# Optimization experiments

Measured on AMD Instinct MI355X. Metric: run time of the kernel, lower is better.

## Reference

```python
import jax, jax.numpy as jnp
import numpy as np

GAMMA = 1.4
EX = jnp.array([1.0, 0.0], dtype=jnp.float32)
EY = jnp.array([0.0, 1.0], dtype=jnp.float32)


def _mlp(x, Ws, bs):
    h = x
    for W, b in zip(Ws[:-1], bs[:-1]):
        h = jnp.tanh(h @ W + b)
    return h @ Ws[-1] + bs[-1]


def setup_inputs() -> dict:
    key = jax.random.key(0)
    ks = jax.random.split(key, 24)
    N, NB = 32768, 4096
    inp = {}
    dom = jnp.array([1.5, 1.0], dtype=jnp.float32)
    inp['x_train'] = jax.random.uniform(ks[0], (N, 2), dtype=jnp.float32) * dom
    inp['x_inlet'] = jax.random.uniform(ks[1], (NB, 2), dtype=jnp.float32) * dom
    inp['U_inlet'] = jax.random.normal(ks[2], (NB, 4), dtype=jnp.float32)
    inp['x_base'] = jax.random.uniform(ks[3], (NB, 2), dtype=jnp.float32) * dom
    inp['x_top'] = jax.random.uniform(ks[4], (NB, 2), dtype=jnp.float32) * dom
    inp['x_slipNormal'] = jax.random.uniform(ks[5], (NB, 2), dtype=jnp.float32) * dom
    dims = [2, 128, 128, 128, 128, 4]
    for i in range(5):
        fan_in = dims[i]
        inp[f'W{i}'] = jax.random.normal(ks[6 + i], (dims[i], dims[i + 1]), dtype=jnp.float32) / jnp.sqrt(jnp.float32(fan_in))
        inp[f'b{i}'] = jnp.zeros((dims[i + 1],), dtype=jnp.float32)
    d2 = [2, 64, 64, 1]
    for i in range(3):
        inp[f'V{i}'] = jax.random.normal(ks[12 + i], (d2[i], d2[i + 1]), dtype=jnp.float32) / jnp.sqrt(jnp.float32(d2[i]))
        inp[f'c{i}'] = jnp.zeros((d2[i + 1],), dtype=jnp.float32)
    return inp


def reference(x_train, x_inlet, U_inlet, x_base, x_top, x_slipNormal,
              W0, b0, W1, b1, W2, b2, W3, b3, W4, b4,
              V0, c0, V1, c1, V2, c2):
    Ws = [W0, W1, W2, W3, W4]
    bs = [b0, b1, b2, b3, b4]
    Vs = [V0, V1, V2]
    cs = [c0, c1, c2]

    def fields(xy):
        # per-point: returns [U1..U4, f1..f4, g1..g4] (12,)
        rho, p, u, v = _mlp(xy, Ws, bs)
        E = p / (GAMMA - 1.0) + 0.5 * rho * (u * u + v * v)
        return jnp.stack([
            rho, rho * u, rho * v, E,                               # U
            rho * u, rho * u * u + p, rho * u * v, u * (E + p),     # f (x-flux)
            rho * v, rho * u * v, rho * v * v + p, v * (E + p)])    # g (y-flux)

    def dUx(xy):
        return jax.jvp(fields, (xy,), (EX,))[1][:4]

    def dUy(xy):
        return jax.jvp(fields, (xy,), (EY,))[1][:4]

    def point_residual(xy):
        _, dx = jax.jvp(fields, (xy,), (EX,))   # x-derivs of all 12 fields
        _, dy = jax.jvp(fields, (xy,), (EY,))   # y-derivs
        U_xx = jax.jvp(dUx, (xy,), (EX,))[1]    # second derivs (fwd-over-fwd)
        U_yy = jax.jvp(dUy, (xy,), (EY,))[1]
        mu = 0.01 * _mlp(xy, Vs, cs)[0] ** 2
        res = dx[4:8] + dy[8:12] - mu * (U_xx + U_yy)  # (4,)
        return res, mu

    res, mu = jax.vmap(point_residual)(x_train)  # res: (N,4), mu: (N,)
    physics = jnp.sum(jnp.mean(res ** 2, axis=0))  # r1+r2+r3+r4

    out_in = _mlp(x_inlet, Ws, bs)
    inlet = jnp.sum(jnp.mean((out_in - U_inlet) ** 2, axis=0))

    base = jnp.mean(_mlp(x_base, Ws, bs)[:, 3] ** 2)
    top = jnp.mean(_mlp(x_top, Ws, bs)[:, 3] ** 2)

    ang = -jnp.pi / 18.0
    o = _mlp(x_slipNormal, Ws, bs)
    slip = jnp.mean((-o[:, 2] * jnp.sin(ang) + o[:, 3] * jnp.cos(ang)) ** 2)

    total = physics + 10.0 * (inlet + base + top + slip) + 0.1 * jnp.mean(mu ** 2)
    return total
```

## Files before the change

### kernel.cpp

```cpp
#include <hip/hip_runtime.h>

#define NTRAIN 32768
#define NBDY   4096
#define PHYS_BLOCKS (NTRAIN / 32)
#define BDY_BLOCKS  256

typedef _Float16 f16x8 __attribute__((ext_vector_type(8)));
typedef __fp16   fp16x2 __attribute__((ext_vector_type(2)));
typedef float    f32x4 __attribute__((ext_vector_type(4)));

union FragU { uint4 q; f16x8 b; _Float16 e[8]; };
union F4  { float4 v; float f[4]; };
union U2h { _Float16 e[4]; uint2 d; };
union H2  { fp16x2 h; _Float16 e[2]; unsigned int u; };

__device__ __forceinline__ float fast_tanh(float z) {
    float e = __expf(2.0f * z);
    return 1.0f - 2.0f * __builtin_amdgcn_rcpf(e + 1.0f);
}

__device__ __forceinline__ unsigned int pk2(float a, float b) {
    H2 r; r.h = __builtin_amdgcn_cvt_pkrtz(a, b);
    return r.u;
}

__global__ __launch_bounds__(256) void pack_w_kernel(
    const float* __restrict__ W1, const float* __restrict__ W2,
    const float* __restrict__ W3, const float* __restrict__ V1,
    const float* __restrict__ W4,
    unsigned short* __restrict__ wsU, float* __restrict__ out)
{
    int b = blockIdx.x;
    if (b < 24) {
        int mat = b >> 3, rb = b & 7;
        const float* W = (mat == 0) ? W1 : (mat == 1) ? W2 : W3;
        unsigned int* hiU = (unsigned int*)(wsU + mat * 32768);
        unsigned int* loU = hiU + 8192;
        int n   = threadIdx.x & 127;
        int pr0 = threadIdx.x >> 7;
        #pragma unroll
        for (int it = 0; it < 4; it++) {
            int pr = pr0 + 2 * it;
            int k  = rb * 16 + pr * 2;
            float v0 = W[k * 128 + n];
            float v1 = W[(k + 1) * 128 + n];
            H2 hh, ll;
            hh.e[0] = (_Float16)v0;
            hh.e[1] = (_Float16)v1;
            ll.e[0] = (_Float16)(v0 - (float)hh.e[0]);
            ll.e[1] = (_Float16)(v1 - (float)hh.e[1]);
            int base = ((n >> 4) * 4 + (k >> 5)) * 64 + ((k >> 3) & 3) * 16 + (n & 15);
            int uoff = base * 4 + ((k & 7) >> 1);
            hiU[uoff] = hh.u;
            loU[uoff] = ll.u;
        }
    } else if (b == 24) {
        unsigned int* hiU = (unsigned int*)(wsU + 98304);
        int n   = threadIdx.x & 63;
        int pr0 = threadIdx.x >> 6;
        #pragma unroll
        for (int it = 0; it < 8; it++) {
            int pr = pr0 + 4 * it;
            int k  = pr * 2;
            float v0 = V1[k * 64 + n];
            float v1 = V1[(k + 1) * 64 + n];
            H2 hh;
            hh.e[0] = (_Float16)v0;
            hh.e[1] = (_Float16)v1;
            int base = ((n >> 4) * 2 + (k >> 5)) * 64 + ((k >> 3) & 3) * 16 + (n & 15);
            hiU[base * 4 + ((k & 7) >> 1)] = hh.u;
        }
        if (threadIdx.x == 0) out[0] = 0.f;
    } else {
        _Float16* hi = (_Float16*)(wsU + 102400);
        _Float16* lo = hi + 2048;
        int u4 = threadIdx.x;
        int lane = u4 & 63, ks = u4 >> 6;
        int m  = lane & 15;
        int kb = ks * 32 + ((lane >> 4) << 3);
        FragU fh, fl;
        #pragma unroll
        for (int j = 0; j < 8; j++) {
            float v = (m < 4) ? W4[(kb + j) * 4 + m] : 0.f;
            _Float16 h = (_Float16)v;
            fh.e[j] = h;
            fl.e[j] = (_Float16)(v - (float)h);
        }
        *(uint4*)(hi + u4 * 8) = fh.q;
        *(uint4*)(lo + u4 * 8) = fl.q;
    }
}

__global__ __launch_bounds__(256, 4) void fused_kernel(
    const float* __restrict__ xt,
    const float* __restrict__ x_inlet, const float* __restrict__ U_inlet,
    const float* __restrict__ x_base,  const float* __restrict__ x_top,
    const float* __restrict__ x_slip,
    const float* __restrict__ W0, const float* __restrict__ b0,
    const float* __restrict__ W1, const float* __restrict__ b1,
    const float* __restrict__ W2, const float* __restrict__ b2,
    const float* __restrict__ W3, const float* __restrict__ b3,
    const float* __restrict__ W4, const float* __restrict__ b4,
    const float* __restrict__ V0, const float* __restrict__ c0,
    const float* __restrict__ V1, const float* __restrict__ c1,
    const float* __restrict__ V2, const float* __restrict__ c2,
    const unsigned short* __restrict__ wsU,
    float* __restrict__ out)
{
    __shared__ float SM[9664];
    const int t = threadIdx.x;
    const int wv   = t >> 6;
    const int lane = t & 63;
    const int nn   = lane & 15;
    const int q    = lane >> 4;

    if (blockIdx.x < PHYS_BLOCKS) {
        unsigned short* AhU = (unsigned short*)SM;
        float* OUTF   = SM + 8704;
        float* MUPART = SM + 9216;
        float* BIASF  = SM + 9280;

        if (t < 128) {
            BIASF[t]       = b1[t];
            BIASF[128 + t] = b2[t];
            BIASF[256 + t] = b3[t];
        }

        {
            const int g = wv >> 1, h = wv & 1;
            const float2 xyn = *(const float2*)(xt + (blockIdx.x * 32 + g * 16 + nn) * 2);
            FragU mb[2];
            #pragma unroll
            for (int ks = 0; ks < 2; ks++) {
                int u0 = ks * 32 + q * 8;
                F4 va0, va1, vb0, vb1, cc0, cc1;
                va0.v = *(const float4*)(V0 + u0);
                va1.v = *(const float4*)(V0 + u0 + 4);
                vb0.v = *(const float4*)(V0 + 64 + u0);
                vb1.v = *(const float4*)(V0 + 64 + u0 + 4);
                cc0.v = *(const float4*)(c0 + u0);
                cc1.v = *(const float4*)(c0 + u0 + 4);
                #pragma unroll
                for (int i = 0; i < 4; i++) {
                    mb[ks].e[i]     = (_Float16)fast_tanh(
                        xyn.x * va0.f[i] + xyn.y * vb0.f[i] + cc0.f[i]);
                    mb[ks].e[4 + i] = (_Float16)fast_tanh(
                        xyn.x * va1.f[i] + xyn.y * vb1.f[i] + cc1.f[i]);
                }
            }
            float partial = 0.f;
            #pragma unroll
            for (int i = 0; i < 2; i++) {
                f32x4 macc = {0.f, 0.f, 0.f, 0.f};
                #pragma unroll
                for (int ks = 0; ks < 2; ks++) {
                    FragU vh;
                    vh.q = *(const uint4*)(wsU + 98304 +
                           ((((2 * h + i) * 2 + ks) * 64 + lane) << 3));
                    macc = __builtin_amdgcn_mfma_f32_16x16x32_f16(vh.b, mb[ks].b, macc, 0, 0, 0);
                }
                int u2 = (2 * h + i) * 16 + q * 4;
                F4 cv, w2;
                cv.v = *(const float4*)(c1 + u2);
                w2.v = *(const float4*)(V2 + u2);
                #pragma unroll
                for (int r = 0; r < 4; r++)
                    partial += fast_tanh(macc[r] + cv.f[r]) * w2.f[r];
            }
            partial += __shfl_xor(partial, 16);
            partial += __shfl_xor(partial, 32);
            if (lane < 16) MUPART[wv * 16 + nn] = partial;
        }
        {
            const int pl = t >> 4, c = t & 15;
            #pragma unroll
            for (int h = 0; h < 2; h++) {
                const int p = h * 16 + pl;
                const float2 xy = *(const float2*)(xt + (blockIdx.x * 32 + p) * 2);
                const float x = xy.x, y = xy.y;
                float vals[4][8];
                #pragma unroll
                for (int j = 0; j < 8; j++) {
                    int u = c * 8 + j;
                    float w0 = W0[u], w1 = W0[128 + u];
                    float zv = x * w0 + y * w1 + b0[u];
                    float tt = fast_tanh(zv);
                    float s2 = 1.f - tt * tt;
                    float m2 = -2.f * tt * s2;
                    vals[0][j] = tt;
                    vals[1][j] = s2 * w0;
                    vals[2][j] = s2 * w1;
                    vals[3][j] = m2 * (w0 * w0 + w1 * w1);
                }
                #pragma unroll
                for (int s = 0; s < 4; s++) {
                    uint4 d = make_uint4(pk2(vals[s][0], vals[s][1]),
                                         pk2(vals[s][2], vals[s][3]),
                                         pk2(vals[s][4], vals[s][5]),
                                         pk2(vals[s][6], vals[s][7]));
                    *(uint4*)(AhU + ((h * 4 + s) * 16 + pl) * 136 + c * 8) = d;
                }
            }
        }
        __syncthreads();

        #pragma unroll 1
        for (int l = 0; l < 3; l++) {
            const unsigned short* WpL = wsU + l * 32768;
            f32x4 acc[2][8];
            #pragma unroll
            for (int i = 0; i < 2; i++)
                #pragma unroll
                for (int s = 0; s < 8; s++) {
                    acc[i][s][0] = 0.f; acc[i][s][1] = 0.f;
                    acc[i][s][2] = 0.f; acc[i][s][3] = 0.f;
                }
            #pragma unroll
            for (int ks = 0; ks < 4; ks++) {
                FragU wh[2];
                #pragma unroll
                for (int i = 0; i < 2; i++)
                    wh[i].q = *(const uint4*)(WpL + ((((2 * wv + i) * 4 + ks) * 64 + lane) << 3));
                #pragma unroll
                for (int s = 0; s < 8; s++) {
                    FragU bh;
                    bh.q = *(const uint4*)(AhU + (s * 16 + nn) * 136 + ks * 32 + q * 8);
                    acc[0][s] = __builtin_amdgcn_mfma_f32_16x16x32_f16(
                        wh[0].b, bh.b, acc[0][s], 0, 0, 0);
                    acc[1][s] = __builtin_amdgcn_mfma_f32_16x16x32_f16(
                        wh[1].b, bh.b, acc[1][s], 0, 0, 0);
                }
            }
            __syncthreads();
            #pragma unroll
            for (int i = 0; i < 2; i++) {
                const int ubase = (2 * wv + i) * 16 + q * 4;
                F4 bv; bv.v = *(const float4*)&BIASF[l * 128 + ubase];
                #pragma unroll
                for (int g = 0; g < 2; g++) {
                    float vals[4][4];
                    #pragma unroll
                    for (int r = 0; r < 4; r++) {
                        float z  = acc[i][g * 4 + 0][r] + bv.f[r];
                        float zx = acc[i][g * 4 + 1][r];
                        float zy = acc[i][g * 4 + 2][r];
                        float zl = acc[i][g * 4 + 3][r];
                        float tt = fast_tanh(z);
                        float s2 = 1.f - tt * tt;
                        float m2 = -2.f * tt * s2;
                        vals[0][r] = tt;
                        vals[1][r] = s2 * zx;
                        vals[2][r] = s2 * zy;
                        vals[3][r] = s2 * zl + m2 * (zx * zx + zy * zy);
                    }
                    #pragma unroll
                    for (int s = 0; s < 4; s++) {
                        uint2 d = make_uint2(pk2(vals[s][0], vals[s][1]),
                                             pk2(vals[s][2], vals[s][3]));
                        *(uint2*)(AhU + ((g * 4 + s) * 16 + nn) * 136 + ubase) = d;
                    }
                }
            }
            __syncthreads();
        }

        {
            const unsigned short* W4p = wsU + 102400;
            #pragma unroll
            for (int g = 0; g < 2; g++) {
                const int rt = g * 4 + wv;
                f32x4 a4 = {0.f, 0.f, 0.f, 0.f};
                #pragma unroll
                for (int ks = 0; ks < 4; ks++) {
                    FragU bh, wh, wl;
                    bh.q = *(const uint4*)(AhU + (rt * 16 + nn) * 136 + ks * 32 + q * 8);
                    const unsigned short* base = W4p + ((ks * 64 + lane) << 3);
                    wh.q = *(const uint4*)base;
                    wl.q = *(const uint4*)(base + 2048);
                    a4 = __builtin_amdgcn_mfma_f32_16x16x32_f16(wh.b, bh.b, a4, 0, 0, 0);
                    a4 = __builtin_amdgcn_mfma_f32_16x16x32_f16(wl.b, bh.b, a4, 0, 0, 0);
                }
                if (q == 0) {
                    float4 o = make_float4(a4[0], a4[1], a4[2], a4[3]);
                    if (wv == 0) {
                        o.x += b4[0]; o.y += b4[1]; o.z += b4[2]; o.w += b4[3];
                    }
                    *(float4*)&OUTF[(rt * 16 + nn) * 4] = o;
                }
            }
        }
        __syncthreads();

        float contrib = 0.f;
        if (t < 32) {
            const int pp = t, g = pp >> 4, p15 = pp & 15;
            const float* V   = &OUTF[((g * 4 + 0) * 16 + p15) * 4];
            const float* DX  = &OUTF[((g * 4 + 1) * 16 + p15) * 4];
            const float* DY  = &OUTF[((g * 4 + 2) * 16 + p15) * 4];
            const float* LAP = &OUTF[((g * 4 + 3) * 16 + p15) * 4];
            float r = V[0],  P = V[1],  u = V[2],  v = V[3];
            float rx = DX[0], Px = DX[1], ux = DX[2], vx = DX[3];
            float ry = DY[0], Py = DY[1], uy = DY[2], vy = DY[3];
            float rl = LAP[0], Pl = LAP[1], ul = LAP[2], vl = LAP[3];
            const float GI = 2.5f;

            float s = MUPART[g * 32 + p15] + MUPART[g * 32 + 16 + p15] + c2[0];
            float mu = 0.01f * s * s;

            float q2 = u * u + v * v;
            float E  = P * GI + 0.5f * r * q2;
            float Ex = Px * GI + 0.5f * rx * q2 + r * (u * ux + v * vx);
            float Ey = Py * GI + 0.5f * ry * q2 + r * (u * uy + v * vy);
            float EpP = E + P;

            float f1x = rx * u + r * ux;
            float f2x = rx * u * u + 2.f * r * u * ux + Px;
            float f3x = rx * u * v + r * ux * v + r * u * vx;
            float f4x = ux * EpP + u * (Ex + Px);

            float g1y = ry * v + r * vy;
            float g2y = ry * u * v + r * uy * v + r * u * vy;
            float g3y = ry * v * v + 2.f * r * v * vy + Py;
            float g4y = vy * EpP + v * (Ey + Py);

            float qx  = 2.f * (u * ux + v * vx);
            float qy  = 2.f * (u * uy + v * vy);
            float ql  = 2.f * (ux * ux + uy * uy + vx * vx + vy * vy)
                      + 2.f * (u * ul + v * vl);

            float U1s = rl;
            float U2s = rl * u + 2.f * (rx * ux + ry * uy) + r * ul;
            float U3s = rl * v + 2.f * (rx * vx + ry * vy) + r * vl;
            float U4s = Pl * GI
                      + 0.5f * (rl * q2 + 2.f * (rx * qx + ry * qy) + r * ql);

            float r1 = f1x + g1y - mu * U1s;
            float r2 = f2x + g2y - mu * U2s;
            float r3 = f3x + g3y - mu * U3s;
            float r4 = f4x + g4y - mu * U4s;

            contrib = (r1 * r1 + r2 * r2 + r3 * r3 + r4 * r4 + 0.1f * mu * mu)
                      * (1.0f / (float)NTRAIN);
        }
        if (t < 64) {
            contrib += __shfl_down(contrib, 32);
            contrib += __shfl_down(contrib, 16);
            contrib += __shfl_down(contrib, 8);
            contrib += __shfl_down(contrib, 4);
            contrib += __shfl_down(contrib, 2);
            contrib += __shfl_down(contrib, 1);
            if (t == 0) atomicAdd(out, contrib);
        }
    } else {
        unsigned short* ShU = (unsigned short*)SM;
        float* OUTB  = SM + 4352;
        float* BIASB = SM + 4608;

        const int bb    = blockIdx.x - PHYS_BLOCKS;
        const int batch = bb >> 6;
        const int lb    = bb & 63;
        const float* xs = (batch == 0) ? x_inlet
                        : (batch == 1) ? x_base
                        : (batch == 2) ? x_top : x_slip;
        const int base_pt = lb * 64;

        {
            int p2 = t & 63, ug = t >> 6;
            float2 xy = *(const float2*)(xs + (base_pt + p2) * 2);
            float x = xy.x, y = xy.y;
            #pragma unroll
            for (int g = 0; g < 8; g++) {
                int u0 = ug * 32 + g * 4;
                F4 wa, wb, bbv;
                wa.v  = *(const float4*)(W0 + u0);
                wb.v  = *(const float4*)(W0 + 128 + u0);
                bbv.v = *(const float4*)(b0 + u0);
                float t0 = fast_tanh(x * wa.f[0] + y * wb.f[0] + bbv.f[0]);
                float t1 = fast_tanh(x * wa.f[1] + y * wb.f[1] + bbv.f[1]);
                float t2 = fast_tanh(x * wa.f[2] + y * wb.f[2] + bbv.f[2]);
                float t3 = fast_tanh(x * wa.f[3] + y * wb.f[3] + bbv.f[3]);
                uint2 d = make_uint2(pk2(t0, t1), pk2(t2, t3));
                *(uint2*)(ShU + p2 * 136 + u0) = d;
            }
            if (t < 128) {
                BIASB[t]       = b1[t];
                BIASB[128 + t] = b2[t];
                BIASB[256 + t] = b3[t];
            }
        }
        __syncthreads();

        #pragma unroll 1
        for (int l = 0; l < 3; l++) {
            const unsigned short* WpL = wsU + l * 32768;
            f32x4 acc[2][4];
            #pragma unroll
            for (int i = 0; i < 2; i++)
                #pragma unroll
                for (int n = 0; n < 4; n++) {
                    acc[i][n][0] = 0.f; acc[i][n][1] = 0.f;
                    acc[i][n][2] = 0.f; acc[i][n][3] = 0.f;
                }
            #pragma unroll
            for (int ks = 0; ks < 4; ks++) {
                FragU bh[4];
                #pragma unroll
                for (int n = 0; n < 4; n++)
                    bh[n].q = *(const uint4*)(ShU + (n * 16 + nn) * 136 + ks * 32 + q * 8);
                FragU wh[2];
                #pragma unroll
                for (int i = 0; i < 2; i++)
                    wh[i].q = *(const uint4*)(WpL + ((((2 * wv + i) * 4 + ks) * 64 + lane) << 3));
                #pragma unroll
                for (int i = 0; i < 2; i++)
                    #pragma unroll
                    for (int n = 0; n < 4; n++)
                        acc[i][n] = __builtin_amdgcn_mfma_f32_16x16x32_f16(
                            wh[i].b, bh[n].b, acc[i][n], 0, 0, 0);
            }
            __syncthreads();
            #pragma unroll
            for (int i = 0; i < 2; i++) {
                int ubase = (2 * wv + i) * 16 + q * 4;
                F4 bv; bv.v = *(const float4*)&BIASB[l * 128 + ubase];
                #pragma unroll
                for (int n = 0; n < 4; n++) {
                    float t0 = fast_tanh(acc[i][n][0] + bv.f[0]);
                    float t1 = fast_tanh(acc[i][n][1] + bv.f[1]);
                    float t2 = fast_tanh(acc[i][n][2] + bv.f[2]);
                    float t3 = fast_tanh(acc[i][n][3] + bv.f[3]);
                    uint2 d = make_uint2(pk2(t0, t1), pk2(t2, t3));
                    *(uint2*)(ShU + (n * 16 + nn) * 136 + ubase) = d;
                }
            }
            __syncthreads();
        }

        {
            const unsigned short* W4p = wsU + 102400;
            f32x4 a4 = {0.f, 0.f, 0.f, 0.f};
            #pragma unroll
            for (int ks = 0; ks < 4; ks++) {
                FragU bh, wh, wl;
                bh.q = *(const uint4*)(ShU + (wv * 16 + nn) * 136 + ks * 32 + q * 8);
                const unsigned short* base = W4p + ((ks * 64 + lane) << 3);
                wh.q = *(const uint4*)base;
                wl.q = *(const uint4*)(base + 2048);
                a4 = __builtin_amdgcn_mfma_f32_16x16x32_f16(wh.b, bh.b, a4, 0, 0, 0);
                a4 = __builtin_amdgcn_mfma_f32_16x16x32_f16(wl.b, bh.b, a4, 0, 0, 0);
            }
            if (q == 0) {
                float4 o = make_float4(a4[0] + b4[0], a4[1] + b4[1],
                                       a4[2] + b4[2], a4[3] + b4[3]);
                *(float4*)&OUTB[(wv * 16 + nn) * 4] = o;
            }
        }
        __syncthreads();

        float contrib = 0.f;
        if (t < 64) {
            float o0 = OUTB[t * 4 + 0], o1 = OUTB[t * 4 + 1];
            float o2 = OUTB[t * 4 + 2], o3 = OUTB[t * 4 + 3];
            float l;
            if (batch == 0) {
                float4 Ui = *(const float4*)(U_inlet + (base_pt + t) * 4);
                float d0 = o0 - Ui.x, d1 = o1 - Ui.y, d2 = o2 - Ui.z, d3 = o3 - Ui.w;
                l = d0 * d0 + d1 * d1 + d2 * d2 + d3 * d3;
            } else if (batch == 3) {
                const float sa = -0.17364817766693033f;
                const float ca =  0.9848077530122080f;
                float d = -o2 * sa + o3 * ca;
                l = d * d;
            } else {
                l = o3 * o3;
            }
            contrib = 10.0f * l * (1.0f / (float)NBDY);
        }
        if (t < 64) {
            contrib += __shfl_down(contrib, 32);
            contrib += __shfl_down(contrib, 16);
            contrib += __shfl_down(contrib, 8);
            contrib += __shfl_down(contrib, 4);
            contrib += __shfl_down(contrib, 2);
            contrib += __shfl_down(contrib, 1);
            if (t == 0) atomicAdd(out, contrib);
        }
    }
}

extern "C" void kernel_launch(void* const* d_in, const int* in_sizes, int n_in,
                              void* d_out, int out_size, void* d_ws, size_t ws_size,
                              hipStream_t stream) {
    const float* xt      = (const float*)d_in[0];
    const float* x_inlet = (const float*)d_in[1];
    const float* U_inlet = (const float*)d_in[2];
    const float* x_base  = (const float*)d_in[3];
    const float* x_top   = (const float*)d_in[4];
    const float* x_slip  = (const float*)d_in[5];
    const float* W0 = (const float*)d_in[6];
    const float* b0 = (const float*)d_in[7];
    const float* W1 = (const float*)d_in[8];
    const float* b1 = (const float*)d_in[9];
    const float* W2 = (const float*)d_in[10];
    const float* b2 = (const float*)d_in[11];
    const float* W3 = (const float*)d_in[12];
    const float* b3 = (const float*)d_in[13];
    const float* W4 = (const float*)d_in[14];
    const float* b4 = (const float*)d_in[15];
    const float* V0 = (const float*)d_in[16];
    const float* c0 = (const float*)d_in[17];
    const float* V1 = (const float*)d_in[18];
    const float* c1 = (const float*)d_in[19];
    const float* V2 = (const float*)d_in[20];
    const float* c2 = (const float*)d_in[21];
    float* out = (float*)d_out;
    unsigned short* wsU = (unsigned short*)d_ws;

    pack_w_kernel<<<26, 256, 0, stream>>>(W1, W2, W3, V1, W4, wsU, out);

    fused_kernel<<<PHYS_BLOCKS + BDY_BLOCKS, 256, 0, stream>>>(
        xt, x_inlet, U_inlet, x_base, x_top, x_slip,
        W0, b0, W1, b1, W2, b2, W3, b3, W4, b4,
        V0, c0, V1, c1, V2, c2, wsU, out);
}
```

Before: 132.8 us.

## Double block size to 512 threads with 64 points and per-wave weight ownership

```diff
diff --git a/kernel.cpp b/kernel.cpp
--- a/kernel.cpp
+++ b/kernel.cpp
@@ -2,8 +2,10 @@
 
 #define NTRAIN 32768
 #define NBDY   4096
-#define PHYS_BLOCKS (NTRAIN / 32)
-#define BDY_BLOCKS  256
+#define PHYS_BLOCKS (NTRAIN / 64)
+#define BDY_BLOCKS  128
+
+#define LDS_BYTES 71680
 
 typedef _Float16 f16x8 __attribute__((ext_vector_type(8)));
 typedef __fp16   fp16x2 __attribute__((ext_vector_type(2)));
@@ -11,7 +13,6 @@
 
 union FragU { uint4 q; f16x8 b; _Float16 e[8]; };
 union F4  { float4 v; float f[4]; };
-union U2h { _Float16 e[4]; uint2 d; };
 union H2  { fp16x2 h; _Float16 e[2]; unsigned int u; };
 
 __device__ __forceinline__ float fast_tanh(float z) {
@@ -91,7 +92,7 @@
     }
 }
 
-__global__ __launch_bounds__(256, 4) void fused_kernel(
+__global__ __launch_bounds__(512, 4) void fused_kernel(
     const float* __restrict__ xt,
     const float* __restrict__ x_inlet, const float* __restrict__ U_inlet,
     const float* __restrict__ x_base,  const float* __restrict__ x_top,
@@ -107,7 +108,11 @@
     const unsigned short* __restrict__ wsU,
     float* __restrict__ out)
 {
-    __shared__ float SM[9664];
+    extern __shared__ char SMC[];
+    unsigned short* AhU = (unsigned short*)SMC;
+    float* MUPART = (float*)(SMC + 69632);
+    float* BIASF  = (float*)(SMC + 70144);
+
     const int t = threadIdx.x;
     const int wv   = t >> 6;
     const int lane = t & 63;
@@ -115,10 +120,7 @@
     const int q    = lane >> 4;
 
     if (blockIdx.x < PHYS_BLOCKS) {
-        unsigned short* AhU = (unsigned short*)SM;
-        float* OUTF   = SM + 8704;
-        float* MUPART = SM + 9216;
-        float* BIASF  = SM + 9280;
+        const int blk = blockIdx.x;
 
         if (t < 128) {
             BIASF[t]       = b1[t];
@@ -128,7 +130,7 @@
 
         {
             const int g = wv >> 1, h = wv & 1;
-            const float2 xyn = *(const float2*)(xt + (blockIdx.x * 32 + g * 16 + nn) * 2);
+            const float2 xyn = *(const float2*)(xt + (blk * 64 + g * 16 + nn) * 2);
             FragU mb[2];
             #pragma unroll
             for (int ks = 0; ks < 2; ks++) {
@@ -174,9 +176,9 @@
         {
             const int pl = t >> 4, c = t & 15;
             #pragma unroll
-            for (int h = 0; h < 2; h++) {
-                const int p = h * 16 + pl;
-                const float2 xy = *(const float2*)(xt + (blockIdx.x * 32 + p) * 2);
+            for (int h2 = 0; h2 < 2; h2++) {
+                const int p = h2 * 32 + pl;
+                const float2 xy = *(const float2*)(xt + (blk * 64 + p) * 2);
                 const float x = xy.x, y = xy.y;
                 float vals[4][8];
                 #pragma unroll
@@ -192,13 +194,14 @@
                     vals[2][j] = s2 * w1;
                     vals[3][j] = m2 * (w0 * w0 + w1 * w1);
                 }
+                const int g = p >> 4, p15 = p & 15;
                 #pragma unroll
                 for (int s = 0; s < 4; s++) {
                     uint4 d = make_uint4(pk2(vals[s][0], vals[s][1]),
                                          pk2(vals[s][2], vals[s][3]),
                                          pk2(vals[s][4], vals[s][5]),
                                          pk2(vals[s][6], vals[s][7]));
-                    *(uint4*)(AhU + ((h * 4 + s) * 16 + pl) * 136 + c * 8) = d;
+                    *(uint4*)(AhU + ((g * 4 + s) * 16 + p15) * 136 + c * 8) = d;
                 }
             }
         }
@@ -207,58 +210,51 @@
         #pragma unroll 1
         for (int l = 0; l < 3; l++) {
             const unsigned short* WpL = wsU + l * 32768;
-            f32x4 acc[2][8];
-            #pragma unroll
-            for (int i = 0; i < 2; i++)
-                #pragma unroll
-                for (int s = 0; s < 8; s++) {
-                    acc[i][s][0] = 0.f; acc[i][s][1] = 0.f;
-                    acc[i][s][2] = 0.f; acc[i][s][3] = 0.f;
-                }
+            f32x4 acc[16];
+            #pragma unroll
+            for (int s = 0; s < 16; s++) {
+                acc[s][0] = 0.f; acc[s][1] = 0.f;
+                acc[s][2] = 0.f; acc[s][3] = 0.f;
+            }
+            FragU wh[4];
+            #pragma unroll
+            for (int ks = 0; ks < 4; ks++)
+                wh[ks].q = *(const uint4*)(WpL + (((wv * 4 + ks) * 64 + lane) << 3));
             #pragma unroll
             for (int ks = 0; ks < 4; ks++) {
-                FragU wh[2];
-                #pragma unroll
-                for (int i = 0; i < 2; i++)
-                    wh[i].q = *(const uint4*)(WpL + ((((2 * wv + i) * 4 + ks) * 64 + lane) << 3));
-                #pragma unroll
-                for (int s = 0; s < 8; s++) {
+                #pragma unroll
+                for (int s = 0; s < 16; s++) {
                     FragU bh;
                     bh.q = *(const uint4*)(AhU + (s * 16 + nn) * 136 + ks * 32 + q * 8);
-                    acc[0][s] = __builtin_amdgcn_mfma_f32_16x16x32_f16(
-                        wh[0].b, bh.b, acc[0][s], 0, 0, 0);
-                    acc[1][s] = __builtin_amdgcn_mfma_f32_16x16x32_f16(
-                        wh[1].b, bh.b, acc[1][s], 0, 0, 0);
+                    acc[s] = __builtin_amdgcn_mfma_f32_16x16x32_f16(
+                        wh[ks].b, bh.b, acc[s], 0, 0, 0);
                 }
             }
             __syncthreads();
-            #pragma unroll
-            for (int i = 0; i < 2; i++) {
-                const int ubase = (2 * wv + i) * 16 + q * 4;
-                F4 bv; bv.v = *(const float4*)&BIASF[l * 128 + ubase];
-                #pragma unroll
-                for (int g = 0; g < 2; g++) {
-                    float vals[4][4];
-                    #pragma unroll
-                    for (int r = 0; r < 4; r++) {
-                        float z  = acc[i][g * 4 + 0][r] + bv.f[r];
-                        float zx = acc[i][g * 4 + 1][r];
-                        float zy = acc[i][g * 4 + 2][r];
-                        float zl = acc[i][g * 4 + 3][r];
-                        float tt = fast_tanh(z);
-                        float s2 = 1.f - tt * tt;
-                        float m2 = -2.f * tt * s2;
-                        vals[0][r] = tt;
-                        vals[1][r] = s2 * zx;
-                        vals[2][r] = s2 * zy;
-                        vals[3][r] = s2 * zl + m2 * (zx * zx + zy * zy);
-                    }
-                    #pragma unroll
-                    for (int s = 0; s < 4; s++) {
-                        uint2 d = make_uint2(pk2(vals[s][0], vals[s][1]),
-                                             pk2(vals[s][2], vals[s][3]));
-                        *(uint2*)(AhU + ((g * 4 + s) * 16 + nn) * 136 + ubase) = d;
-                    }
+            const int ubase = wv * 16 + q * 4;
+            F4 bv; bv.v = *(const float4*)&BIASF[l * 128 + ubase];
+            #pragma unroll
+            for (int g = 0; g < 4; g++) {
+                float vals[4][4];
+                #pragma unroll
+                for (int r = 0; r < 4; r++) {
+                    float z  = acc[g * 4 + 0][r] + bv.f[r];
+                    float zx = acc[g * 4 + 1][r];
+                    float zy = acc[g * 4 + 2][r];
+                    float zl = acc[g * 4 + 3][r];
+                    float tt = fast_tanh(z);
+                    float s2 = 1.f - tt * tt;
+                    float m2 = -2.f * tt * s2;
+                    vals[0][r] = tt;
+                    vals[1][r] = s2 * zx;
+                    vals[2][r] = s2 * zy;
+                    vals[3][r] = s2 * zl + m2 * (zx * zx + zy * zy);
+                }
+                #pragma unroll
+                for (int s = 0; s < 4; s++) {
+                    uint2 d = make_uint2(pk2(vals[s][0], vals[s][1]),
+                                         pk2(vals[s][2], vals[s][3]));
+                    *(uint2*)(AhU + ((g * 4 + s) * 16 + nn) * 136 + ubase) = d;
                 }
             }
             __syncthreads();
@@ -266,45 +262,53 @@
 
         {
             const unsigned short* W4p = wsU + 102400;
-            #pragma unroll
-            for (int g = 0; g < 2; g++) {
-                const int rt = g * 4 + wv;
-                f32x4 a4 = {0.f, 0.f, 0.f, 0.f};
-                #pragma unroll
-                for (int ks = 0; ks < 4; ks++) {
-                    FragU bh, wh, wl;
-                    bh.q = *(const uint4*)(AhU + (rt * 16 + nn) * 136 + ks * 32 + q * 8);
-                    const unsigned short* base = W4p + ((ks * 64 + lane) << 3);
-                    wh.q = *(const uint4*)base;
-                    wl.q = *(const uint4*)(base + 2048);
-                    a4 = __builtin_amdgcn_mfma_f32_16x16x32_f16(wh.b, bh.b, a4, 0, 0, 0);
-                    a4 = __builtin_amdgcn_mfma_f32_16x16x32_f16(wl.b, bh.b, a4, 0, 0, 0);
-                }
-                if (q == 0) {
-                    float4 o = make_float4(a4[0], a4[1], a4[2], a4[3]);
-                    if (wv == 0) {
-                        o.x += b4[0]; o.y += b4[1]; o.z += b4[2]; o.w += b4[3];
-                    }
-                    *(float4*)&OUTF[(rt * 16 + nn) * 4] = o;
-                }
+            const int rtA = wv, rtB = 8 + wv;
+            f32x4 aA = {0.f, 0.f, 0.f, 0.f};
+            f32x4 aB = {0.f, 0.f, 0.f, 0.f};
+            #pragma unroll
+            for (int ks = 0; ks < 4; ks++) {
+                FragU wh, wl, bA, bB;
+                const unsigned short* base = W4p + ((ks * 64 + lane) << 3);
+                wh.q = *(const uint4*)base;
+                wl.q = *(const uint4*)(base + 2048);
+                bA.q = *(const uint4*)(AhU + (rtA * 16 + nn) * 136 + ks * 32 + q * 8);
+                bB.q = *(const uint4*)(AhU + (rtB * 16 + nn) * 136 + ks * 32 + q * 8);
+                aA = __builtin_amdgcn_mfma_f32_16x16x32_f16(wh.b, bA.b, aA, 0, 0, 0);
+                aA = __builtin_amdgcn_mfma_f32_16x16x32_f16(wl.b, bA.b, aA, 0, 0, 0);
+                aB = __builtin_amdgcn_mfma_f32_16x16x32_f16(wh.b, bB.b, aB, 0, 0, 0);
+                aB = __builtin_amdgcn_mfma_f32_16x16x32_f16(wl.b, bB.b, aB, 0, 0, 0);
+            }
+            if (q == 0) {
+                float4 oA = make_float4(aA[0], aA[1], aA[2], aA[3]);
+                float4 oB = make_float4(aB[0], aB[1], aB[2], aB[3]);
+                if ((rtA & 3) == 0) {
+                    oA.x += b4[0]; oA.y += b4[1]; oA.z += b4[2]; oA.w += b4[3];
+                }
+                if ((rtB & 3) == 0) {
+                    oB.x += b4[0]; oB.y += b4[1]; oB.z += b4[2]; oB.w += b4[3];
+                }
+                *(float4*)(SMC + (rtA * 16 + nn) * 272 + 256) = oA;
+                *(float4*)(SMC + (rtB * 16 + nn) * 272 + 256) = oB;
             }
         }
         __syncthreads();
 
         float contrib = 0.f;
-        if (t < 32) {
+        if (t < 64) {
             const int pp = t, g = pp >> 4, p15 = pp & 15;
-            const float* V   = &OUTF[((g * 4 + 0) * 16 + p15) * 4];
-            const float* DX  = &OUTF[((g * 4 + 1) * 16 + p15) * 4];
-            const float* DY  = &OUTF[((g * 4 + 2) * 16 + p15) * 4];
-            const float* LAP = &OUTF[((g * 4 + 3) * 16 + p15) * 4];
-            float r = V[0],  P = V[1],  u = V[2],  v = V[3];
-            float rx = DX[0], Px = DX[1], ux = DX[2], vx = DX[3];
-            float ry = DY[0], Py = DY[1], uy = DY[2], vy = DY[3];
-            float rl = LAP[0], Pl = LAP[1], ul = LAP[2], vl = LAP[3];
+            F4 V, DX, DY, LAP;
+            V.v   = *(const float4*)(SMC + ((g * 4 + 0) * 16 + p15) * 272 + 256);
+            DX.v  = *(const float4*)(SMC + ((g * 4 + 1) * 16 + p15) * 272 + 256);
+            DY.v  = *(const float4*)(SMC + ((g * 4 + 2) * 16 + p15) * 272 + 256);
+            LAP.v = *(const float4*)(SMC + ((g * 4 + 3) * 16 + p15) * 272 + 256);
+            float r = V.f[0],  P = V.f[1],  u = V.f[2],  v = V.f[3];
+            float rx = DX.f[0], Px = DX.f[1], ux = DX.f[2], vx = DX.f[3];
+            float ry = DY.f[0], Py = DY.f[1], uy = DY.f[2], vy = DY.f[3];
+            float rl = LAP.f[0], Pl = LAP.f[1], ul = LAP.f[2], vl = LAP.f[3];
             const float GI = 2.5f;
 
-            float s = MUPART[g * 32 + p15] + MUPART[g * 32 + 16 + p15] + c2[0];
+            float s = MUPART[(2 * g) * 16 + p15] + MUPART[(2 * g + 1) * 16 + p15]
+                    + c2[0];
             float mu = 0.01f * s * s;
 
             float q2 = u * u + v * v;
@@ -352,20 +356,16 @@
             if (t == 0) atomicAdd(out, contrib);
         }
     } else {
-        unsigned short* ShU = (unsigned short*)SM;
-        float* OUTB  = SM + 4352;
-        float* BIASB = SM + 4608;
-
         const int bb    = blockIdx.x - PHYS_BLOCKS;
-        const int batch = bb >> 6;
-        const int lb    = bb & 63;
+        const int batch = bb >> 5;
+        const int lb    = bb & 31;
         const float* xs = (batch == 0) ? x_inlet
                         : (batch == 1) ? x_base
                         : (batch == 2) ? x_top : x_slip;
-        const int base_pt = lb * 64;
+        const int base_pt = lb * 128;
 
         {
-            int p2 = t & 63, ug = t >> 6;
+            int p2 = t & 127, ug = t >> 7;
             float2 xy = *(const float2*)(xs + (base_pt + p2) * 2);
             float x = xy.x, y = xy.y;
             #pragma unroll
@@ -380,12 +380,12 @@
                 float t2 = fast_tanh(x * wa.f[2] + y * wb.f[2] + bbv.f[2]);
                 float t3 = fast_tanh(x * wa.f[3] + y * wb.f[3] + bbv.f[3]);
                 uint2 d = make_uint2(pk2(t0, t1), pk2(t2, t3));
-                *(uint2*)(ShU + p2 * 136 + u0) = d;
+                *(uint2*)(AhU + p2 * 136 + u0) = d;
             }
             if (t < 128) {
-                BIASB[t]       = b1[t];
-                BIASB[128 + t] = b2[t];
-                BIASB[256 + t] = b3[t];
+                BIASF[t]       = b1[t];
+                BIASF[128 + t] = b2[t];
+                BIASF[256 + t] = b3[t];
             }
         }
         __syncthreads();
@@ -393,45 +393,37 @@
         #pragma unroll 1
         for (int l = 0; l < 3; l++) {
             const unsigned short* WpL = wsU + l * 32768;
-            f32x4 acc[2][4];
-            #pragma unroll
-            for (int i = 0; i < 2; i++)
-                #pragma unroll
-                for (int n = 0; n < 4; n++) {
-                    acc[i][n][0] = 0.f; acc[i][n][1] = 0.f;
-                    acc[i][n][2] = 0.f; acc[i][n][3] = 0.f;
-                }
+            f32x4 acc[8];
+            #pragma unroll
+            for (int n = 0; n < 8; n++) {
+                acc[n][0] = 0.f; acc[n][1] = 0.f;
+                acc[n][2] = 0.f; acc[n][3] = 0.f;
+            }
+            FragU wh[4];
+            #pragma unroll
+            for (int ks = 0; ks < 4; ks++)
+                wh[ks].q = *(const uint4*)(WpL + (((wv * 4 + ks) * 64 + lane) << 3));
             #pragma unroll
             for (int ks = 0; ks < 4; ks++) {
-                FragU bh[4];
-                #pragma unroll
-                for (int n = 0; n < 4; n++)
-                    bh[n].q = *(const uint4*)(ShU + (n * 16 + nn) * 136 + ks * 32 + q * 8);
-                FragU wh[2];
-                #pragma unroll
-                for (int i = 0; i < 2; i++)
-                    wh[i].q = *(const uint4*)(WpL + ((((2 * wv + i) * 4 + ks) * 64 + lane) << 3));
-                #pragma unroll
-                for (int i = 0; i < 2; i++)
-                    #pragma unroll
-                    for (int n = 0; n < 4; n++)
-                        acc[i][n] = __builtin_amdgcn_mfma_f32_16x16x32_f16(
-                            wh[i].b, bh[n].b, acc[i][n], 0, 0, 0);
+                #pragma unroll
+                for (int n = 0; n < 8; n++) {
+                    FragU bh;
+                    bh.q = *(const uint4*)(AhU + (n * 16 + nn) * 136 + ks * 32 + q * 8);
+                    acc[n] = __builtin_amdgcn_mfma_f32_16x16x32_f16(
+                        wh[ks].b, bh.b, acc[n], 0, 0, 0);
+                }
             }
             __syncthreads();
-            #pragma unroll
-            for (int i = 0; i < 2; i++) {
-                int ubase = (2 * wv + i) * 16 + q * 4;
-                F4 bv; bv.v = *(const float4*)&BIASB[l * 128 + ubase];
-                #pragma unroll
-                for (int n = 0; n < 4; n++) {
-                    float t0 = fast_tanh(acc[i][n][0] + bv.f[0]);
-                    float t1 = fast_tanh(acc[i][n][1] + bv.f[1]);
-                    float t2 = fast_tanh(acc[i][n][2] + bv.f[2]);
-                    float t3 = fast_tanh(acc[i][n][3] + bv.f[3]);
-                    uint2 d = make_uint2(pk2(t0, t1), pk2(t2, t3));
-                    *(uint2*)(ShU + (n * 16 + nn) * 136 + ubase) = d;
-                }
+            const int ubase = wv * 16 + q * 4;
+            F4 bv; bv.v = *(const float4*)&BIASF[l * 128 + ubase];
+            #pragma unroll
+            for (int n = 0; n < 8; n++) {
+                float t0 = fast_tanh(acc[n][0] + bv.f[0]);
+                float t1 = fast_tanh(acc[n][1] + bv.f[1]);
+                float t2 = fast_tanh(acc[n][2] + bv.f[2]);
+                float t3 = fast_tanh(acc[n][3] + bv.f[3]);
+                uint2 d = make_uint2(pk2(t0, t1), pk2(t2, t3));
+                *(uint2*)(AhU + (n * 16 + nn) * 136 + ubase) = d;
             }
             __syncthreads();
         }
@@ -442,7 +434,7 @@
             #pragma unroll
             for (int ks = 0; ks < 4; ks++) {
                 FragU bh, wh, wl;
-                bh.q = *(const uint4*)(ShU + (wv * 16 + nn) * 136 + ks * 32 + q * 8);
+                bh.q = *(const uint4*)(AhU + (wv * 16 + nn) * 136 + ks * 32 + q * 8);
                 const unsigned short* base = W4p + ((ks * 64 + lane) << 3);
                 wh.q = *(const uint4*)base;
                 wl.q = *(const uint4*)(base + 2048);
@@ -452,15 +444,14 @@
             if (q == 0) {
                 float4 o = make_float4(a4[0] + b4[0], a4[1] + b4[1],
                                        a4[2] + b4[2], a4[3] + b4[3]);
-                *(float4*)&OUTB[(wv * 16 + nn) * 4] = o;
+                *(float4*)(SMC + (wv * 16 + nn) * 272 + 256) = o;
             }
         }
         __syncthreads();
 
-        float contrib = 0.f;
-        if (t < 64) {
-            float o0 = OUTB[t * 4 + 0], o1 = OUTB[t * 4 + 1];
-            float o2 = OUTB[t * 4 + 2], o3 = OUTB[t * 4 + 3];
+        if (t < 128) {
+            F4 O; O.v = *(const float4*)(SMC + t * 272 + 256);
+            float o0 = O.f[0], o1 = O.f[1], o2 = O.f[2], o3 = O.f[3];
             float l;
             if (batch == 0) {
                 float4 Ui = *(const float4*)(U_inlet + (base_pt + t) * 4);
@@ -474,16 +465,14 @@
             } else {
                 l = o3 * o3;
             }
-            contrib = 10.0f * l * (1.0f / (float)NBDY);
-        }
-        if (t < 64) {
+            float contrib = 10.0f * l * (1.0f / (float)NBDY);
             contrib += __shfl_down(contrib, 32);
             contrib += __shfl_down(contrib, 16);
             contrib += __shfl_down(contrib, 8);
             contrib += __shfl_down(contrib, 4);
             contrib += __shfl_down(contrib, 2);
             contrib += __shfl_down(contrib, 1);
-            if (t == 0) atomicAdd(out, contrib);
+            if ((t & 63) == 0) atomicAdd(out, contrib);
         }
     }
 }
@@ -518,7 +507,10 @@
 
     pack_w_kernel<<<26, 256, 0, stream>>>(W1, W2, W3, V1, W4, wsU, out);
 
-    fused_kernel<<<PHYS_BLOCKS + BDY_BLOCKS, 256, 0, stream>>>(
+    (void)hipFuncSetAttribute((const void*)fused_kernel,
+                              hipFuncAttributeMaxDynamicSharedMemorySize,
+                              LDS_BYTES);
+    fused_kernel<<<PHYS_BLOCKS + BDY_BLOCKS, 512, LDS_BYTES, stream>>>(
         xt, x_inlet, U_inlet, x_base, x_top, x_slip,
         W0, b0, W1, b1, W2, b2, W3, b3, W4, b4,
         V0, c0, V1, c1, V2, c2, wsU, out);
```

Measured after the change: 130.0 us. 2.2% less time.

## Swizzle shared activations, drop bias/output LDS staging, raise occupancy to five blocks

Applied to the files above, without the earlier changes.

```diff
diff --git a/kernel.cpp b/kernel.cpp
--- a/kernel.cpp
+++ b/kernel.cpp
@@ -11,7 +11,6 @@
 
 union FragU { uint4 q; f16x8 b; _Float16 e[8]; };
 union F4  { float4 v; float f[4]; };
-union U2h { _Float16 e[4]; uint2 d; };
 union H2  { fp16x2 h; _Float16 e[2]; unsigned int u; };
 
 __device__ __forceinline__ float fast_tanh(float z) {
@@ -22,6 +21,10 @@
 __device__ __forceinline__ unsigned int pk2(float a, float b) {
     H2 r; r.h = __builtin_amdgcn_cvt_pkrtz(a, b);
     return r.u;
+}
+
+__device__ __forceinline__ int swz(int row, int col) {
+    return (row * 128 + col) ^ ((row & 7) << 3);
 }
 
 __global__ __launch_bounds__(256) void pack_w_kernel(
@@ -91,7 +94,7 @@
     }
 }
 
-__global__ __launch_bounds__(256, 4) void fused_kernel(
+__global__ __launch_bounds__(256, 5) void fused_kernel(
     const float* __restrict__ xt,
     const float* __restrict__ x_inlet, const float* __restrict__ U_inlet,
     const float* __restrict__ x_base,  const float* __restrict__ x_top,
@@ -107,7 +110,7 @@
     const unsigned short* __restrict__ wsU,
     float* __restrict__ out)
 {
-    __shared__ float SM[9664];
+    __shared__ unsigned short AhU[16384];
     const int t = threadIdx.x;
     const int wv   = t >> 6;
     const int lane = t & 63;
@@ -115,20 +118,11 @@
     const int q    = lane >> 4;
 
     if (blockIdx.x < PHYS_BLOCKS) {
-        unsigned short* AhU = (unsigned short*)SM;
-        float* OUTF   = SM + 8704;
-        float* MUPART = SM + 9216;
-        float* BIASF  = SM + 9280;
-
-        if (t < 128) {
-            BIASF[t]       = b1[t];
-            BIASF[128 + t] = b2[t];
-            BIASF[256 + t] = b3[t];
-        }
-
-        {
-            const int g = wv >> 1, h = wv & 1;
-            const float2 xyn = *(const float2*)(xt + (blockIdx.x * 32 + g * 16 + nn) * 2);
+        const int blk = blockIdx.x;
+
+        float mu = 0.f;
+        if (wv < 2) {
+            const float2 xyn = *(const float2*)(xt + (blk * 32 + wv * 16 + nn) * 2);
             FragU mb[2];
             #pragma unroll
             for (int ks = 0; ks < 2; ks++) {
@@ -150,16 +144,16 @@
             }
             float partial = 0.f;
             #pragma unroll
-            for (int i = 0; i < 2; i++) {
+            for (int tu = 0; tu < 4; tu++) {
                 f32x4 macc = {0.f, 0.f, 0.f, 0.f};
                 #pragma unroll
                 for (int ks = 0; ks < 2; ks++) {
                     FragU vh;
                     vh.q = *(const uint4*)(wsU + 98304 +
-                           ((((2 * h + i) * 2 + ks) * 64 + lane) << 3));
+                           (((tu * 2 + ks) * 64 + lane) << 3));
                     macc = __builtin_amdgcn_mfma_f32_16x16x32_f16(vh.b, mb[ks].b, macc, 0, 0, 0);
                 }
-                int u2 = (2 * h + i) * 16 + q * 4;
+                int u2 = tu * 16 + q * 4;
                 F4 cv, w2;
                 cv.v = *(const float4*)(c1 + u2);
                 w2.v = *(const float4*)(V2 + u2);
@@ -169,14 +163,15 @@
             }
             partial += __shfl_xor(partial, 16);
             partial += __shfl_xor(partial, 32);
-            if (lane < 16) MUPART[wv * 16 + nn] = partial;
+            float s = partial + c2[0];
+            mu = 0.01f * s * s;
         }
         {
             const int pl = t >> 4, c = t & 15;
             #pragma unroll
-            for (int h = 0; h < 2; h++) {
-                const int p = h * 16 + pl;
-                const float2 xy = *(const float2*)(xt + (blockIdx.x * 32 + p) * 2);
+            for (int h2 = 0; h2 < 2; h2++) {
+                const int p = h2 * 16 + pl;
+                const float2 xy = *(const float2*)(xt + (blk * 32 + p) * 2);
                 const float x = xy.x, y = xy.y;
                 float vals[4][8];
                 #pragma unroll
@@ -198,7 +193,7 @@
                                          pk2(vals[s][2], vals[s][3]),
                                          pk2(vals[s][4], vals[s][5]),
                                          pk2(vals[s][6], vals[s][7]));
-                    *(uint4*)(AhU + ((h * 4 + s) * 16 + pl) * 136 + c * 8) = d;
+                    *(uint4*)(AhU + swz((h2 * 4 + s) * 16 + pl, c * 8)) = d;
                 }
             }
         }
@@ -207,6 +202,7 @@
         #pragma unroll 1
         for (int l = 0; l < 3; l++) {
             const unsigned short* WpL = wsU + l * 32768;
+            const float* bl = (l == 0) ? b1 : (l == 1) ? b2 : b3;
             f32x4 acc[2][8];
             #pragma unroll
             for (int i = 0; i < 2; i++)
@@ -224,7 +220,7 @@
                 #pragma unroll
                 for (int s = 0; s < 8; s++) {
                     FragU bh;
-                    bh.q = *(const uint4*)(AhU + (s * 16 + nn) * 136 + ks * 32 + q * 8);
+                    bh.q = *(const uint4*)(AhU + swz(s * 16 + nn, ks * 32 + q * 8));
                     acc[0][s] = __builtin_amdgcn_mfma_f32_16x16x32_f16(
                         wh[0].b, bh.b, acc[0][s], 0, 0, 0);
                     acc[1][s] = __builtin_amdgcn_mfma_f32_16x16x32_f16(
@@ -235,7 +231,7 @@
             #pragma unroll
             for (int i = 0; i < 2; i++) {
                 const int ubase = (2 * wv + i) * 16 + q * 4;
-                F4 bv; bv.v = *(const float4*)&BIASF[l * 128 + ubase];
+                F4 bv; bv.v = *(const float4*)(bl + ubase);
                 #pragma unroll
                 for (int g = 0; g < 2; g++) {
                     float vals[4][4];
@@ -257,105 +253,87 @@
                     for (int s = 0; s < 4; s++) {
                         uint2 d = make_uint2(pk2(vals[s][0], vals[s][1]),
                                              pk2(vals[s][2], vals[s][3]));
-                        *(uint2*)(AhU + ((g * 4 + s) * 16 + nn) * 136 + ubase) = d;
+                        *(uint2*)(AhU + swz((g * 4 + s) * 16 + nn, ubase)) = d;
                     }
                 }
             }
             __syncthreads();
         }
 
-        {
+        if (wv < 2) {
             const unsigned short* W4p = wsU + 102400;
-            #pragma unroll
-            for (int g = 0; g < 2; g++) {
-                const int rt = g * 4 + wv;
-                f32x4 a4 = {0.f, 0.f, 0.f, 0.f};
-                #pragma unroll
-                for (int ks = 0; ks < 4; ks++) {
-                    FragU bh, wh, wl;
-                    bh.q = *(const uint4*)(AhU + (rt * 16 + nn) * 136 + ks * 32 + q * 8);
-                    const unsigned short* base = W4p + ((ks * 64 + lane) << 3);
-                    wh.q = *(const uint4*)base;
-                    wl.q = *(const uint4*)(base + 2048);
-                    a4 = __builtin_amdgcn_mfma_f32_16x16x32_f16(wh.b, bh.b, a4, 0, 0, 0);
-                    a4 = __builtin_amdgcn_mfma_f32_16x16x32_f16(wl.b, bh.b, a4, 0, 0, 0);
-                }
-                if (q == 0) {
-                    float4 o = make_float4(a4[0], a4[1], a4[2], a4[3]);
-                    if (wv == 0) {
-                        o.x += b4[0]; o.y += b4[1]; o.z += b4[2]; o.w += b4[3];
-                    }
-                    *(float4*)&OUTF[(rt * 16 + nn) * 4] = o;
-                }
-            }
-        }
-        __syncthreads();
-
-        float contrib = 0.f;
-        if (t < 32) {
-            const int pp = t, g = pp >> 4, p15 = pp & 15;
-            const float* V   = &OUTF[((g * 4 + 0) * 16 + p15) * 4];
-            const float* DX  = &OUTF[((g * 4 + 1) * 16 + p15) * 4];
-            const float* DY  = &OUTF[((g * 4 + 2) * 16 + p15) * 4];
-            const float* LAP = &OUTF[((g * 4 + 3) * 16 + p15) * 4];
-            float r = V[0],  P = V[1],  u = V[2],  v = V[3];
-            float rx = DX[0], Px = DX[1], ux = DX[2], vx = DX[3];
-            float ry = DY[0], Py = DY[1], uy = DY[2], vy = DY[3];
-            float rl = LAP[0], Pl = LAP[1], ul = LAP[2], vl = LAP[3];
-            const float GI = 2.5f;
-
-            float s = MUPART[g * 32 + p15] + MUPART[g * 32 + 16 + p15] + c2[0];
-            float mu = 0.01f * s * s;
-
-            float q2 = u * u + v * v;
-            float E  = P * GI + 0.5f * r * q2;
-            float Ex = Px * GI + 0.5f * rx * q2 + r * (u * ux + v * vx);
-            float Ey = Py * GI + 0.5f * ry * q2 + r * (u * uy + v * vy);
-            float EpP = E + P;
-
-            float f1x = rx * u + r * ux;
-            float f2x = rx * u * u + 2.f * r * u * ux + Px;
-            float f3x = rx * u * v + r * ux * v + r * u * vx;
-            float f4x = ux * EpP + u * (Ex + Px);
-
-            float g1y = ry * v + r * vy;
-            float g2y = ry * u * v + r * uy * v + r * u * vy;
-            float g3y = ry * v * v + 2.f * r * v * vy + Py;
-            float g4y = vy * EpP + v * (Ey + Py);
-
-            float qx  = 2.f * (u * ux + v * vx);
-            float qy  = 2.f * (u * uy + v * vy);
-            float ql  = 2.f * (ux * ux + uy * uy + vx * vx + vy * vy)
-                      + 2.f * (u * ul + v * vl);
-
-            float U1s = rl;
-            float U2s = rl * u + 2.f * (rx * ux + ry * uy) + r * ul;
-            float U3s = rl * v + 2.f * (rx * vx + ry * vy) + r * vl;
-            float U4s = Pl * GI
-                      + 0.5f * (rl * q2 + 2.f * (rx * qx + ry * qy) + r * ql);
-
-            float r1 = f1x + g1y - mu * U1s;
-            float r2 = f2x + g2y - mu * U2s;
-            float r3 = f3x + g3y - mu * U3s;
-            float r4 = f4x + g4y - mu * U4s;
-
-            contrib = (r1 * r1 + r2 * r2 + r3 * r3 + r4 * r4 + 0.1f * mu * mu)
-                      * (1.0f / (float)NTRAIN);
-        }
-        if (t < 64) {
+            f32x4 a4[4];
+            #pragma unroll
+            for (int s = 0; s < 4; s++) {
+                a4[s][0] = 0.f; a4[s][1] = 0.f; a4[s][2] = 0.f; a4[s][3] = 0.f;
+            }
+            #pragma unroll
+            for (int ks = 0; ks < 4; ks++) {
+                FragU wh, wl;
+                const unsigned short* base = W4p + ((ks * 64 + lane) << 3);
+                wh.q = *(const uint4*)base;
+                wl.q = *(const uint4*)(base + 2048);
+                #pragma unroll
+                for (int s = 0; s < 4; s++) {
+                    FragU bh;
+                    bh.q = *(const uint4*)(AhU + swz((wv * 4 + s) * 16 + nn, ks * 32 + q * 8));
+                    a4[s] = __builtin_amdgcn_mfma_f32_16x16x32_f16(wh.b, bh.b, a4[s], 0, 0, 0);
+                    a4[s] = __builtin_amdgcn_mfma_f32_16x16x32_f16(wl.b, bh.b, a4[s], 0, 0, 0);
+                }
+            }
+            float contrib = 0.f;
+            if (q == 0) {
+                float r  = a4[0][0] + b4[0], P = a4[0][1] + b4[1];
+                float u  = a4[0][2] + b4[2], v = a4[0][3] + b4[3];
+                float rx = a4[1][0], Px = a4[1][1], ux = a4[1][2], vx = a4[1][3];
+                float ry = a4[2][0], Py = a4[2][1], uy = a4[2][2], vy = a4[2][3];
+                float rl = a4[3][0], Pl = a4[3][1], ul = a4[3][2], vl = a4[3][3];
+                const float GI = 2.5f;
+
+                float q2 = u * u + v * v;
+                float E  = P * GI + 0.5f * r * q2;
+                float Ex = Px * GI + 0.5f * rx * q2 + r * (u * ux + v * vx);
+                float Ey = Py * GI + 0.5f * ry * q2 + r * (u * uy + v * vy);
+                float EpP = E + P;
+
+                float f1x = rx * u + r * ux;
+                float f2x = rx * u * u + 2.f * r * u * ux + Px;
+                float f3x = rx * u * v + r * ux * v + r * u * vx;
+                float f4x = ux * EpP + u * (Ex + Px);
+
+                float g1y = ry * v + r * vy;
+                float g2y = ry * u * v + r * uy * v + r * u * vy;
+                float g3y = ry * v * v + 2.f * r * v * vy + Py;
+                float g4y = vy * EpP + v * (Ey + Py);
+
+                float qx  = 2.f * (u * ux + v * vx);
+                float qy  = 2.f * (u * uy + v * vy);
+                float ql  = 2.f * (ux * ux + uy * uy + vx * vx + vy * vy)
+                          + 2.f * (u * ul + v * vl);
+
+                float U1s = rl;
+                float U2s = rl * u + 2.f * (rx * ux + ry * uy) + r * ul;
+                float U3s = rl * v + 2.f * (rx * vx + ry * vy) + r * vl;
+                float U4s = Pl * GI
+                          + 0.5f * (rl * q2 + 2.f * (rx * qx + ry * qy) + r * ql);
+
+                float r1 = f1x + g1y - mu * U1s;
+                float r2 = f2x + g2y - mu * U2s;
+                float r3 = f3x + g3y - mu * U3s;
+                float r4 = f4x + g4y - mu * U4s;
+
+                contrib = (r1 * r1 + r2 * r2 + r3 * r3 + r4 * r4 + 0.1f * mu * mu)
+                          * (1.0f / (float)NTRAIN);
+            }
             contrib += __shfl_down(contrib, 32);
             contrib += __shfl_down(contrib, 16);
             contrib += __shfl_down(contrib, 8);
             contrib += __shfl_down(contrib, 4);
             contrib += __shfl_down(contrib, 2);
             contrib += __shfl_down(contrib, 1);
-            if (t == 0) atomicAdd(out, contrib);
+            if (lane == 0) atomicAdd(out, contrib);
         }
     } else {
-        unsigned short* ShU = (unsigned short*)SM;
-        float* OUTB  = SM + 4352;
-        float* BIASB = SM + 4608;
-
         const int bb    = blockIdx.x - PHYS_BLOCKS;
         const int batch = bb >> 6;
         const int lb    = bb & 63;
@@ -380,12 +358,7 @@
                 float t2 = fast_tanh(x * wa.f[2] + y * wb.f[2] + bbv.f[2]);
                 float t3 = fast_tanh(x * wa.f[3] + y * wb.f[3] + bbv.f[3]);
                 uint2 d = make_uint2(pk2(t0, t1), pk2(t2, t3));
-                *(uint2*)(ShU + p2 * 136 + u0) = d;
-            }
-            if (t < 128) {
-                BIASB[t]       = b1[t];
-                BIASB[128 + t] = b2[t];
-                BIASB[256 + t] = b3[t];
+                *(uint2*)(AhU + swz(p2, u0)) = d;
             }
         }
         __syncthreads();
@@ -393,6 +366,7 @@
         #pragma unroll 1
         for (int l = 0; l < 3; l++) {
             const unsigned short* WpL = wsU + l * 32768;
+            const float* bl = (l == 0) ? b1 : (l == 1) ? b2 : b3;
             f32x4 acc[2][4];
             #pragma unroll
             for (int i = 0; i < 2; i++)
@@ -406,7 +380,7 @@
                 FragU bh[4];
                 #pragma unroll
                 for (int n = 0; n < 4; n++)
-                    bh[n].q = *(const uint4*)(ShU + (n * 16 + nn) * 136 + ks * 32 + q * 8);
+                    bh[n].q = *(const uint4*)(AhU + swz(n * 16 + nn, ks * 32 + q * 8));
                 FragU wh[2];
                 #pragma unroll
                 for (int i = 0; i < 2; i++)
@@ -422,7 +396,7 @@
             #pragma unroll
             for (int i = 0; i < 2; i++) {
                 int ubase = (2 * wv + i) * 16 + q * 4;
-                F4 bv; bv.v = *(const float4*)&BIASB[l * 128 + ubase];
+                F4 bv; bv.v = *(const float4*)(bl + ubase);
                 #pragma unroll
                 for (int n = 0; n < 4; n++) {
                     float t0 = fast_tanh(acc[i][n][0] + bv.f[0]);
@@ -430,7 +404,7 @@
                     float t2 = fast_tanh(acc[i][n][2] + bv.f[2]);
                     float t3 = fast_tanh(acc[i][n][3] + bv.f[3]);
                     uint2 d = make_uint2(pk2(t0, t1), pk2(t2, t3));
-                    *(uint2*)(ShU + (n * 16 + nn) * 136 + ubase) = d;
+                    *(uint2*)(AhU + swz(n * 16 + nn, ubase)) = d;
                 }
             }
             __syncthreads();
@@ -442,48 +416,39 @@
             #pragma unroll
             for (int ks = 0; ks < 4; ks++) {
                 FragU bh, wh, wl;
-                bh.q = *(const uint4*)(ShU + (wv * 16 + nn) * 136 + ks * 32 + q * 8);
+                bh.q = *(const uint4*)(AhU + swz(wv * 16 + nn, ks * 32 + q * 8));
                 const unsigned short* base = W4p + ((ks * 64 + lane) << 3);
                 wh.q = *(const uint4*)base;
                 wl.q = *(const uint4*)(base + 2048);
                 a4 = __builtin_amdgcn_mfma_f32_16x16x32_f16(wh.b, bh.b, a4, 0, 0, 0);
                 a4 = __builtin_amdgcn_mfma_f32_16x16x32_f16(wl.b, bh.b, a4, 0, 0, 0);
             }
+            float contrib = 0.f;
             if (q == 0) {
-                float4 o = make_float4(a4[0] + b4[0], a4[1] + b4[1],
-                                       a4[2] + b4[2], a4[3] + b4[3]);
-                *(float4*)&OUTB[(wv * 16 + nn) * 4] = o;
-            }
-        }
-        __syncthreads();
-
-        float contrib = 0.f;
-        if (t < 64) {
-            float o0 = OUTB[t * 4 + 0], o1 = OUTB[t * 4 + 1];
-            float o2 = OUTB[t * 4 + 2], o3 = OUTB[t * 4 + 3];
-            float l;
-            if (batch == 0) {
-                float4 Ui = *(const float4*)(U_inlet + (base_pt + t) * 4);
-                float d0 = o0 - Ui.x, d1 = o1 - Ui.y, d2 = o2 - Ui.z, d3 = o3 - Ui.w;
-                l = d0 * d0 + d1 * d1 + d2 * d2 + d3 * d3;
-            } else if (batch == 3) {
-                const float sa = -0.17364817766693033f;
-                const float ca =  0.9848077530122080f;
-                float d = -o2 * sa + o3 * ca;
-                l = d * d;
-            } else {
-                l = o3 * o3;
-            }
-            contrib = 10.0f * l * (1.0f / (float)NBDY);
-        }
-        if (t < 64) {
+                float o0 = a4[0] + b4[0], o1 = a4[1] + b4[1];
+                float o2 = a4[2] + b4[2], o3 = a4[3] + b4[3];
+                float l;
+                if (batch == 0) {
+                    float4 Ui = *(const float4*)(U_inlet + (base_pt + wv * 16 + nn) * 4);
+                    float d0 = o0 - Ui.x, d1 = o1 - Ui.y, d2 = o2 - Ui.z, d3 = o3 - Ui.w;
+                    l = d0 * d0 + d1 * d1 + d2 * d2 + d3 * d3;
+                } else if (batch == 3) {
+                    const float sa = -0.17364817766693033f;
+                    const float ca =  0.9848077530122080f;
+                    float d = -o2 * sa + o3 * ca;
+                    l = d * d;
+                } else {
+                    l = o3 * o3;
+                }
+                contrib = 10.0f * l * (1.0f / (float)NBDY);
+            }
             contrib += __shfl_down(contrib, 32);
             contrib += __shfl_down(contrib, 16);
             contrib += __shfl_down(contrib, 8);
             contrib += __shfl_down(contrib, 4);
             contrib += __shfl_down(contrib, 2);
             contrib += __shfl_down(contrib, 1);
-            if (t == 0) atomicAdd(out, contrib);
+            if (lane == 0) atomicAdd(out, contrib);
         }
     }
 }
```

Result: slower. 200.3 us (+50.8%).
